# Optimization experiments

Measured on AMD Instinct MI355X. Metric: run time of the kernel, lower is better.

## Reference

```python
import jax, jax.numpy as jnp
import numpy as np

AGENT_RADIUS = 0.2
SAFETY_DIST = 0.1
_ang = np.linspace(0.0, 2.0 * np.pi, 8, endpoint=False)
OBSTACLES = np.stack([10.0 * np.cos(_ang), 10.0 * np.sin(_ang), 0.5 * np.ones(8)], axis=-1).astype(np.float32)  # (x, y, r)


def _qp_solve(p, G, h):
    """Exact solve of: min_z 0.5 z^T z + p^T z  s.t. G z <= h, z in R^2.
    Equivalent to QPFunction with Q=I. Enumerates KKT candidates over active
    sets of size 0, 1, 2 (closed form in 2D) and picks the feasible optimum.
    p: [2], G: [m,2], h: [m]."""
    m = G.shape[0]
    ii, jj = np.triu_indices(m, 1)
    # active set {} -> unconstrained minimizer
    z0 = -p[None, :]                                        # [1,2]
    # active set {i}: z = -p - lam*g_i, g_i.z = h_i
    gg = jnp.sum(G * G, axis=-1)                            # [m]
    lam1 = (-(G @ p) - h) / (gg + 1e-12)
    z1 = -p[None, :] - lam1[:, None] * G                    # [m,2]
    ok1 = lam1 >= -1e-8
    # active set {i,j}: z solves 2x2 system [g_i; g_j] z = [h_i; h_j]
    Gi, Gj = G[ii], G[jj]                                   # [P,2]
    hi, hj = h[ii], h[jj]
    det = Gi[:, 0] * Gj[:, 1] - Gi[:, 1] * Gj[:, 0]
    det_ok = jnp.abs(det) > 1e-9
    ds = jnp.where(det_ok, det, 1.0)
    zx = (hi * Gj[:, 1] - hj * Gi[:, 1]) / ds
    zy = (Gi[:, 0] * hj - Gj[:, 0] * hi) / ds
    z2 = jnp.stack([zx, zy], axis=-1)                       # [P,2]
    r = -(z2 + p[None, :])                                  # A^T lam = r
    lam_i = (Gj[:, 1] * r[:, 0] - Gj[:, 0] * r[:, 1]) / ds
    lam_j = (Gi[:, 0] * r[:, 1] - Gi[:, 1] * r[:, 0]) / ds
    ok2 = det_ok & (lam_i >= -1e-8) & (lam_j >= -1e-8)
    Z = jnp.concatenate([z0, z1, z2], axis=0)               # [K,2]
    ok = jnp.concatenate([jnp.ones((1,), bool), ok1, ok2], axis=0)
    tol = 1e-6 * (1.0 + jnp.abs(h))
    feas = jnp.all(Z @ G.T <= (h + tol)[None, :], axis=-1)  # [K]
    obj = 0.5 * jnp.sum(Z * Z, axis=-1) + Z @ p
    obj = jnp.where(ok & feas, obj, jnp.inf)
    return Z[jnp.argmin(obj)]


def _forward(x, mean, std, W1, b1, W21, b21, W31, b31, W22, b22, W32, b32):
    x0 = x * std + mean                                     # de-normalized state [B,8]
    hid = jax.nn.relu(x @ W1.T + b1)
    x31 = jax.nn.relu(hid @ W21.T + b21) @ W31.T + b31      # reference control p [B,2]
    x32 = 4.0 * jax.nn.sigmoid(jax.nn.relu(hid @ W22.T + b22) @ W32.T + b32)  # CBF penalties [B,2]
    px, py, theta, v = x0[:, 0], x0[:, 1], x0[:, 2], x0[:, 3]
    ox, oy, oth, ov = x0[:, 4], x0[:, 5], x0[:, 6], x0[:, 7]
    st, ct = jnp.sin(theta), jnp.cos(theta)
    vs, vc = v * st, v * ct
    obs = jnp.asarray(OBSTACLES, x.dtype)
    # static obstacle constraints, vectorized over the n_obs obstacles
    dx = px[:, None] - obs[None, :, 0]                      # [B,n_obs]
    dy = py[:, None] - obs[None, :, 1]
    R = AGENT_RADIUS + obs[:, 2] + SAFETY_DIST
    bar = dx * dx + dy * dy - (R * R)[None, :]
    bdot = 2.0 * dx * vc[:, None] + 2.0 * dy * vs[:, None]
    Lf2b = (2.0 * v * v)[:, None]
    u1 = -2.0 * dx * vs[:, None] + 2.0 * dy * vc[:, None]
    u2 = 2.0 * dx * ct[:, None] + 2.0 * dy * st[:, None]
    G_obs = -jnp.stack([u1, u2], axis=-1)                   # [B,n_obs,2]
    s0, s1 = x32[:, 0:1], x32[:, 1:2]
    h_obs = Lf2b + (s0 + s1) * bdot + (s0 * s1) * bar       # [B,n_obs]
    # opponent constraint
    Ro = 2.0 * AGENT_RADIUS + SAFETY_DIST
    dxo, dyo = px - ox, py - oy
    so, co = jnp.sin(oth), jnp.cos(oth)
    bar_o = dxo * dxo + dyo * dyo - Ro * Ro
    bdot_o = 2.0 * dxo * (vc - ov * co) + 2.0 * dyo * (vs - ov * so)
    Lf2b_o = 2.0 * (v * v + ov * ov + 2.0 * v * ov * jnp.cos(theta - oth))
    u1o = -2.0 * dxo * vs + 2.0 * dyo * vc
    u2o = 2.0 * dxo * ct + 2.0 * dyo * st
    G_opp = -jnp.stack([u1o, u2o], axis=-1)[:, None, :]     # [B,1,2]
    h_opp = (Lf2b_o + (x32[:, 0] + x32[:, 1]) * bdot_o + x32[:, 0] * x32[:, 1] * bar_o)[:, None]
    G = jnp.concatenate([G_obs, G_opp], axis=1)             # [B,m,2]
    h = jnp.concatenate([h_obs, h_opp], axis=1)             # [B,m]
    return jax.vmap(_qp_solve)(x31, G, h)                   # [B,2]


def setup_inputs() -> dict:
    key = jax.random.key(0)
    ks = jax.random.split(key, 6)
    B, nF, H1, H2 = 65536, 8, 256, 128

    def lin(k, o, i):
        k1, k2 = jax.random.split(k)
        W = jax.random.normal(k1, (o, i), jnp.float32) / np.float32(np.sqrt(i))
        b = jax.random.normal(k2, (o,), jnp.float32) * 0.01
        return W, b

    W1, b1 = lin(ks[0], H1, nF)
    W21, b21 = lin(ks[1], H2, H1)
    W31, b31 = lin(ks[2], 2, H2)
    W22, b22 = lin(ks[3], H2, H1)
    W32, b32 = lin(ks[4], 2, H2)
    x = jax.random.normal(ks[5], (B, nF), jnp.float32)
    return {"x": x, "mean": jnp.zeros((nF,), jnp.float32), "std": jnp.ones((nF,), jnp.float32),
            "W1": W1, "b1": b1, "W21": W21, "b21": b21, "W31": W31, "b31": b31,
            "W22": W22, "b22": b22, "W32": W32, "b32": b32, "sgn": 1}


def reference(x, mean, std, W1, b1, W21, b21, W31, b31, W22, b22, W32, b32, sgn):
    # sgn==1 / training path -> batched differentiable QP solve
    return _forward(x, mean, std, W1, b1, W21, b21, W31, b31, W22, b22, W32, b32)
```

## Files before the change

kernel.cpp:

```cpp
#include <hip/hip_runtime.h>
#include <hip/hip_bf16.h>
#include <math.h>


typedef unsigned int u32;
typedef unsigned long long u64;
typedef unsigned short u16;
typedef __attribute__((ext_vector_type(8))) short short8;
typedef __attribute__((ext_vector_type(4))) float f32x4;
typedef __attribute__((ext_vector_type(16))) float f32x16;
typedef __attribute__((ext_vector_type(2))) float f32x2;
typedef __attribute__((ext_vector_type(4))) u32 u32x4;

union Frag  { short8 v; u32 u[4]; u32x4 q; };
union F8    { long l; u32 u[2]; };

__device__ __forceinline__ f32x16 zero16() {
    f32x16 z = {0.f, 0.f, 0.f, 0.f, 0.f, 0.f, 0.f, 0.f,
                0.f, 0.f, 0.f, 0.f, 0.f, 0.f, 0.f, 0.f};
    return z;
}

#define DMA16(gp, lp)                                                        \
    __builtin_amdgcn_global_load_lds(                                        \
        (const __attribute__((address_space(1))) void*)(gp),                 \
        (__attribute__((address_space(3))) void*)(lp), 16, 0, 0)

__device__ __forceinline__ u32 packbf(float a, float b) {
    float2 f2; f2.x = a; f2.y = b;
    __hip_bfloat162 h = __float22bfloat162_rn(f2);
    union { __hip_bfloat162 h2; u32 u; } cv; cv.h2 = h;
    return cv.u;
}
__device__ __forceinline__ u32 packfp8x4(float a, float b, float c, float d) {
    u32 r = 0;
    r = (u32)__builtin_amdgcn_cvt_pk_fp8_f32(a, b, (int)r, false);
    r = (u32)__builtin_amdgcn_cvt_pk_fp8_f32(c, d, (int)r, true);
    return r;
}

__device__ const float OBX[8] = { 10.f, 7.07106781186547524f, 6.123234e-16f, -7.07106781186547524f,
                                 -10.f, -7.07106781186547524f, -1.8369702e-15f, 7.07106781186547524f };
__device__ const float OBY[8] = { 0.f, 7.07106781186547524f, 10.f, 7.07106781186547524f,
                                  1.2246468e-15f, -7.07106781186547524f, -10.f, -7.07106781186547524f };

#define PI0_ 0x2111111100000000ULL
#define PI1_ 0x5544443333322222ULL
#define PI2_ 0x7665ULL
#define PJ0_ 0x3876543287654321ULL
#define PJ1_ 0x7687658765487654ULL
#define PJ2_ 0x8878ULL
__device__ __forceinline__ int unpack4(u64 w0, u64 w1, u64 w2, int t) {
    u64 w = (t < 16) ? w0 : (t < 32) ? w1 : w2;
    return (int)((w >> ((t & 15) * 4)) & 15);
}

__global__ __launch_bounds__(256)
void prep_kernel(const float* __restrict__ W21, const float* __restrict__ W22,
                 const float* __restrict__ W1,  const float* __restrict__ b1,
                 const float* __restrict__ W31, const float* __restrict__ W32,
                 const float* __restrict__ b21, const float* __restrict__ b22,
                 u32* __restrict__ ws)
{
    int idx = blockIdx.x * 256 + threadIdx.x;
    if (idx < 4096) {
        int lane = idx & 63;
        int nt   = (idx >> 6) & 3;
        int kp   = (idx >> 8) & 7;
        int head = idx >> 11;
        const float* W = head ? W22 : W21;
        int o  = nt * 32 + (lane & 31);
        int hi = lane >> 5;
        const float* base = W + o * 256 + kp * 32 + hi * 4;
        u32x4 e;
        e.x = packfp8x4(base[0],  base[1],  base[2],  base[3]);
        e.y = packfp8x4(base[8],  base[9],  base[10], base[11]);
        e.z = packfp8x4(base[16], base[17], base[18], base[19]);
        e.w = packfp8x4(base[24], base[25], base[26], base[27]);
        __builtin_nontemporal_store(e, (u32x4*)ws + idx);
    } else if (idx < 4608) {
        int f = idx - 4096;
        int inst = f >> 6, lane = f & 63;
        int hi = lane >> 5;
        int h  = inst * 32 + (lane & 31);
        u32x4 e = (u32x4){0u, 0u, 0u, 0u};
        if (hi == 0) {
            const float* wr = W1 + h * 8;
            e.x = packbf(wr[0], wr[1]);
            e.y = packbf(wr[2], wr[3]);
            e.z = packbf(wr[4], wr[5]);
            e.w = packbf(wr[6], wr[7]);
        } else {
            e.x = packbf(b1[h], 0.f);
        }
        __builtin_nontemporal_store(e, (u32x4*)ws + idx);
    } else if (idx < 5632) {
        int f = idx - 4608;
        int head = f >> 9;
        int kb   = (f >> 6) & 7;
        int lane = f & 63;
        int hi = lane >> 5;
        int mr = lane & 31;
        const float* W3 = head ? W32 : W31;
        int ob = 32 * (kb >> 1) + 16 * (kb & 1) + 4 * hi;
        float v0=0, v1=0, v2=0, v3=0, v4=0, v5=0, v6=0, v7=0;
        if (mr < 2) {
            const float* wr = W3 + mr * 128;
            v0 = wr[ob];     v1 = wr[ob + 1]; v2 = wr[ob + 2]; v3 = wr[ob + 3];
            v4 = wr[ob + 8]; v5 = wr[ob + 9]; v6 = wr[ob + 10]; v7 = wr[ob + 11];
        }
        u32x4 e;
        e.x = packbf(v0, v1); e.y = packbf(v2, v3);
        e.z = packbf(v4, v5); e.w = packbf(v6, v7);
        __builtin_nontemporal_store(e, (u32x4*)ws + idx);
    } else if (idx < 5696) {
        int f = idx - 5632;
        int head = f >> 5, hi = (f >> 4) & 1, nt = (f >> 2) & 3, t = f & 3;
        const float* b2 = head ? b22 : b21;
        int o0 = nt * 32 + 8 * t + 4 * hi;
        f32x4 e; e.x = b2[o0]; e.y = b2[o0+1]; e.z = b2[o0+2]; e.w = b2[o0+3];
        union { f32x4 f; u32x4 u; } cv; cv.f = e;
        __builtin_nontemporal_store(cv.u, (u32x4*)ws + idx);
    }
}

__global__ __launch_bounds__(256)
void barriernet_kernel(const float* __restrict__ x,
                       const float* __restrict__ meanp,
                       const float* __restrict__ stdp,
                       const float* __restrict__ b31,
                       const float* __restrict__ b32,
                       const u32* __restrict__ wsB,
                       float* __restrict__ out, int Btot)
{
    const int tid  = threadIdx.x;
    const int wave = tid >> 6;
    const int lane = tid & 63;
    const int hi   = lane >> 5;
    const int ml   = lane & 31;
    const int blockRow = blockIdx.x * 128;

    __shared__ u32x4 stage[4096];
    __shared__ float lds_p[128][4];

    const u32x4* wsB4 = (const u32x4*)wsB;

    {
        const u32x4* g0 = wsB4 + wave * 1024 + lane;
        u32x4* l0 = stage + wave * 1024;
        #pragma unroll
        for (int i = 0; i < 16; ++i)
            DMA16(g0 + i * 64, l0 + i * 64);
    }

    Frag xB;
    {
        int R0 = blockRow + wave * 32 + ml;
        const f32x4* xv0 = (const f32x4*)(x + (R0 < Btot ? R0 : 0) * 8);
        f32x4 xa0 = xv0[0], xb0 = xv0[1];
        if (hi == 0) {
            xB.u[0] = packbf(xa0.x, xa0.y);
            xB.u[1] = packbf(xa0.z, xa0.w);
            xB.u[2] = packbf(xb0.x, xb0.y);
            xB.u[3] = packbf(xb0.z, xb0.w);
        } else {
            xB.u[0] = 0x00003f80u;
            xB.u[1] = 0u; xB.u[2] = 0u; xB.u[3] = 0u;
        }
    }
    F8 B8[16];
    #pragma unroll
    for (int chunk = 0; chunk < 2; ++chunk) {
        f32x16 hacc[4];
        #pragma unroll
        for (int i2 = 0; i2 < 4; ++i2) {
            int inst = chunk * 4 + i2;
            Frag W1f; W1f.q = wsB4[4096 + inst * 64 + lane];
            hacc[i2] = __builtin_amdgcn_mfma_f32_32x32x16_bf16(
                W1f.v, xB.v, zero16(), 0, 0, 0);
        }
        #pragma unroll
        for (int k2 = 0; k2 < 8; ++k2) {
            int ks = chunk * 8 + k2;
            int i2 = k2 >> 1;
            int pb = 8 * (k2 & 1);
            B8[ks].u[0] = packfp8x4(fmaxf(hacc[i2][pb+0], 0.f), fmaxf(hacc[i2][pb+1], 0.f),
                                    fmaxf(hacc[i2][pb+2], 0.f), fmaxf(hacc[i2][pb+3], 0.f));
            B8[ks].u[1] = packfp8x4(fmaxf(hacc[i2][pb+4], 0.f), fmaxf(hacc[i2][pb+5], 0.f),
                                    fmaxf(hacc[i2][pb+6], 0.f), fmaxf(hacc[i2][pb+7], 0.f));
        }
    }

    __syncthreads();

    #pragma unroll 1
    for (int head = 0; head < 2; ++head) {
        f32x16 acc[4];
        #pragma unroll
        for (int nt = 0; nt < 4; ++nt) acc[nt] = zero16();

        const u32x4* hS = stage + head * 2048;
        #pragma unroll
        for (int kp = 0; kp < 8; ++kp) {
            #pragma unroll
            for (int nt = 0; nt < 4; ++nt) {
                u32x4 e = hS[kp * 256 + nt * 64 + lane];
                F8 ae; ae.u[0] = e.x; ae.u[1] = e.y;
                F8 ao; ao.u[0] = e.z; ao.u[1] = e.w;
                acc[nt] = __builtin_amdgcn_mfma_f32_32x32x16_fp8_fp8(
                    ae.l, B8[2 * kp].l, acc[nt], 0, 0, 0);
                acc[nt] = __builtin_amdgcn_mfma_f32_32x32x16_fp8_fp8(
                    ao.l, B8[2 * kp + 1].l, acc[nt], 0, 0, 0);
            }
        }

        const f32x4* b2p = (const f32x4*)(wsB4 + 5632 + head * 32 + hi * 16);
        Frag rvB[8];
        #pragma unroll
        for (int nt = 0; nt < 4; ++nt) {
            f32x4 bq0 = b2p[nt * 4 + 0];
            f32x4 bq1 = b2p[nt * 4 + 1];
            f32x4 bq2 = b2p[nt * 4 + 2];
            f32x4 bq3 = b2p[nt * 4 + 3];
            float rv0  = fmaxf(acc[nt][0]  + bq0.x, 0.f);
            float rv1  = fmaxf(acc[nt][1]  + bq0.y, 0.f);
            float rv2  = fmaxf(acc[nt][2]  + bq0.z, 0.f);
            float rv3  = fmaxf(acc[nt][3]  + bq0.w, 0.f);
            float rv4  = fmaxf(acc[nt][4]  + bq1.x, 0.f);
            float rv5  = fmaxf(acc[nt][5]  + bq1.y, 0.f);
            float rv6  = fmaxf(acc[nt][6]  + bq1.z, 0.f);
            float rv7  = fmaxf(acc[nt][7]  + bq1.w, 0.f);
            float rv8  = fmaxf(acc[nt][8]  + bq2.x, 0.f);
            float rv9  = fmaxf(acc[nt][9]  + bq2.y, 0.f);
            float rv10 = fmaxf(acc[nt][10] + bq2.z, 0.f);
            float rv11 = fmaxf(acc[nt][11] + bq2.w, 0.f);
            float rv12 = fmaxf(acc[nt][12] + bq3.x, 0.f);
            float rv13 = fmaxf(acc[nt][13] + bq3.y, 0.f);
            float rv14 = fmaxf(acc[nt][14] + bq3.z, 0.f);
            float rv15 = fmaxf(acc[nt][15] + bq3.w, 0.f);
            rvB[nt * 2 + 0].u[0] = packbf(rv0,  rv1);
            rvB[nt * 2 + 0].u[1] = packbf(rv2,  rv3);
            rvB[nt * 2 + 0].u[2] = packbf(rv4,  rv5);
            rvB[nt * 2 + 0].u[3] = packbf(rv6,  rv7);
            rvB[nt * 2 + 1].u[0] = packbf(rv8,  rv9);
            rvB[nt * 2 + 1].u[1] = packbf(rv10, rv11);
            rvB[nt * 2 + 1].u[2] = packbf(rv12, rv13);
            rvB[nt * 2 + 1].u[3] = packbf(rv14, rv15);
        }
        f32x16 acc3 = zero16();
        #pragma unroll
        for (int kb = 0; kb < 8; ++kb) {
            Frag W3f; W3f.q = wsB4[4608 + head * 512 + kb * 64 + lane];
            acc3 = __builtin_amdgcn_mfma_f32_32x32x16_bf16(
                W3f.v, rvB[kb].v, acc3, 0, 0, 0);
        }
        if (hi == 0) {
            int row = wave * 32 + ml;
            if (head == 0) {
                lds_p[row][0] = acc3[0] + b31[0];
                lds_p[row][1] = acc3[1] + b31[1];
            } else {
                float a0 = acc3[0] + b32[0];
                float a1 = acc3[1] + b32[1];
                lds_p[row][2] = 4.f / (1.f + __expf(-a0));
                lds_p[row][3] = 4.f / (1.f + __expf(-a1));
            }
        }
    }
    __syncthreads();

    f32x4 (*qC)[128]  = (f32x4(*)[128])stage;
    f32x4 (*res)[128] = (f32x4(*)[128])(stage + 1152);

    const int rq   = tid & 127;
    const int part = tid >> 7;
    const int R    = blockRow + rq;
    float p0 = lds_p[rq][0];
    float p1 = lds_p[rq][1];

    {
        float s0 = lds_p[rq][2];
        float s1 = lds_p[rq][3];
        const float* xp = x + (R < Btot ? R : 0) * 8;
        f32x4 xv0 = ((const f32x4*)xp)[0];
        f32x4 xv1 = ((const f32x4*)xp)[1];
        const f32x4 sd0 = ((const f32x4*)stdp)[0],  sd1 = ((const f32x4*)stdp)[1];
        const f32x4 mn0 = ((const f32x4*)meanp)[0], mn1 = ((const f32x4*)meanp)[1];
        float px = fmaf(xv0.x, sd0.x, mn0.x);
        float py = fmaf(xv0.y, sd0.y, mn0.y);
        float th = fmaf(xv0.z, sd0.z, mn0.z);
        float v  = fmaf(xv0.w, sd0.w, mn0.w);
        float st = __sinf(th), ct = __cosf(th);
        float vs = v * st, vc = v * ct;
        float sps = s0 + s1, ss = s0 * s1;
        float Lf2b = 2.f * v * v;
        #pragma unroll
        for (int kk = 0; kk < 4; ++kk) {
            int k = part * 4 + kk;
            float dx = px - OBX[k], dy = py - OBY[k];
            float bar  = dx * dx + dy * dy - 0.64f;
            float bdot = 2.f * dx * vc + 2.f * dy * vs;
            float gx = 2.f * dx * vs - 2.f * dy * vc;
            float gy = -(2.f * dx * ct + 2.f * dy * st);
            float hk = Lf2b + sps * bdot + ss * bar;
            float ht = hk + 1e-6f * (1.f + fabsf(hk));
            qC[k][rq] = (f32x4){gx, gy, hk, ht};
        }
        if (part == 1) {
            float ox = fmaf(xv1.x, sd1.x, mn1.x);
            float oy = fmaf(xv1.y, sd1.y, mn1.y);
            float oth= fmaf(xv1.z, sd1.z, mn1.z);
            float ov = fmaf(xv1.w, sd1.w, mn1.w);
            float so = __sinf(oth), co = __cosf(oth);
            float dxo = px - ox, dyo = py - oy;
            float bar_o  = dxo * dxo + dyo * dyo - 0.25f;
            float bdot_o = 2.f * dxo * (vc - ov * co) + 2.f * dyo * (vs - ov * so);
            float Lf2b_o = 2.f * (v * v + ov * ov + 2.f * v * ov * __cosf(th - oth));
            float gx = 2.f * dxo * vs - 2.f * dyo * vc;
            float gy = -(2.f * dxo * ct + 2.f * dyo * st);
            float hk = Lf2b_o + sps * bdot_o + ss * bar_o;
            float ht = hk + 1e-6f * (1.f + fabsf(hk));
            qC[8][rq] = (f32x4){gx, gy, hk, ht};
        }
    }
    __syncthreads();

    const f32x4 C0 = qC[0][rq], C1 = qC[1][rq], C2 = qC[2][rq];
    const f32x4 C3 = qC[3][rq], C4 = qC[4][rq], C5 = qC[5][rq];
    const f32x4 C6 = qC[6][rq], C7 = qC[7][rq], C8 = qC[8][rq];

    const float zx0 = -p0, zy0 = -p1;
    bool z0ok =
        (zx0 * C0.x + zy0 * C0.y <= C0.w) &&
        (zx0 * C1.x + zy0 * C1.y <= C1.w) &&
        (zx0 * C2.x + zy0 * C2.y <= C2.w) &&
        (zx0 * C3.x + zy0 * C3.y <= C3.w) &&
        (zx0 * C4.x + zy0 * C4.y <= C4.w) &&
        (zx0 * C5.x + zy0 * C5.y <= C5.w) &&
        (zx0 * C6.x + zy0 * C6.y <= C6.w) &&
        (zx0 * C7.x + zy0 * C7.y <= C7.w) &&
        (zx0 * C8.x + zy0 * C8.y <= C8.w);

    float bobj = INFINITY;
    float bzx = zx0, bzy = zy0;
    if (z0ok) {
        if (part == 0)
            bobj = 0.5f * (zx0 * zx0 + zy0 * zy0) + zx0 * p0 + zy0 * p1;
    } else {
        const int c0i = part ? 24 : 0;
        const int c1i = part ? 46 : 24;
        #pragma unroll 2
        for (int c = c0i; c < c1i; ++c) {
            float zx, zy;
            bool pre;
            if (c == 0) {
                zx = -p0; zy = -p1; pre = true;
            } else if (c <= 9) {
                f32x4 g = qC[c - 1][rq];
                float gg  = g.x * g.x + g.y * g.y;
                float lam = (-(g.x * p0 + g.y * p1) - g.z) / (gg + 1e-12f);
                zx = -p0 - lam * g.x;
                zy = -p1 - lam * g.y;
                pre = (lam >= -1e-8f);
            } else {
                int t = c - 10;
                int pi = unpack4(PI0_, PI1_, PI2_, t);
                int pj = unpack4(PJ0_, PJ1_, PJ2_, t);
                f32x4 gi = qC[pi][rq];
                f32x4 gj = qC[pj][rq];
                float det = gi.x * gj.y - gi.y * gj.x;
                bool dok = fabsf(det) > 1e-9f;
                float ds = dok ? det : 1.0f;
                float inv = 1.0f / ds;
                zx = (gi.z * gj.y - gj.z * gi.y) * inv;
                zy = (gi.x * gj.z - gj.x * gi.z) * inv;
                float rx = -(zx + p0), ry = -(zy + p1);
                float li = (gj.y * rx - gj.x * ry) * inv;
                float lj = (gi.x * ry - gi.y * rx) * inv;
                pre = dok && (li >= -1e-8f) && (lj >= -1e-8f);
            }
            bool ok = pre;
            ok = ok && (zx * C0.x + zy * C0.y <= C0.w);
            ok = ok && (zx * C1.x + zy * C1.y <= C1.w);
            ok = ok && (zx * C2.x + zy * C2.y <= C2.w);
            ok = ok && (zx * C3.x + zy * C3.y <= C3.w);
            ok = ok && (zx * C4.x + zy * C4.y <= C4.w);
            ok = ok && (zx * C5.x + zy * C5.y <= C5.w);
            ok = ok && (zx * C6.x + zy * C6.y <= C6.w);
            ok = ok && (zx * C7.x + zy * C7.y <= C7.w);
            ok = ok && (zx * C8.x + zy * C8.y <= C8.w);
            float obj = 0.5f * (zx * zx + zy * zy) + zx * p0 + zy * p1;
            if (ok && obj < bobj) { bobj = obj; bzx = zx; bzy = zy; }
        }
    }

    if (part) {
        res[0][rq] = (f32x4){bobj, bzx, bzy, 0.f};
    }
    __syncthreads();
    if (part == 0) {
        f32x4 r = res[0][rq];
        if (r.x < bobj) { bobj = r.x; bzx = r.y; bzy = r.z; }
        if (R < Btot) {
            f32x2 o2; o2.x = bzx; o2.y = bzy;
            ((f32x2*)out)[R] = o2;
        }
    }
}

extern "C" void kernel_launch(void* const* d_in, const int* in_sizes, int n_in,
                              void* d_out, int out_size, void* d_ws, size_t ws_size,
                              hipStream_t stream) {
    const float* x    = (const float*)d_in[0];
    const float* mean = (const float*)d_in[1];
    const float* stdv = (const float*)d_in[2];
    const float* W1   = (const float*)d_in[3];
    const float* b1   = (const float*)d_in[4];
    const float* W21  = (const float*)d_in[5];
    const float* b21  = (const float*)d_in[6];
    const float* W31  = (const float*)d_in[7];
    const float* b31  = (const float*)d_in[8];
    const float* W22  = (const float*)d_in[9];
    const float* b22  = (const float*)d_in[10];
    const float* W32  = (const float*)d_in[11];
    const float* b32  = (const float*)d_in[12];
    int B = in_sizes[0] / 8;
    float* out = (float*)d_out;
    u32* ws = (u32*)d_ws;

    hipLaunchKernelGGL(prep_kernel, dim3(24), dim3(256), 0, stream,
                       W21, W22, W1, b1, W31, W32, b21, b22, ws);

    hipLaunchKernelGGL(barriernet_kernel, dim3((B + 127) / 128), dim3(256), 0, stream,
                       x, mean, stdv, b31, b32, ws, out, B);
}
```

Baseline: 103.5 us.

## Double block to 512 threads, split heads across waves and QP candidates four ways

Doubles the block size so each row group gets two waves, one per MLP head, instead of one wave looping over both heads. The QP stage is split across four threads per row instead of two, each scanning about a quarter of the candidates, and partial minima are reduced through shared memory. The aim is shorter serial chains per wave and more latency hiding. The cost is that W1 and the first layer are computed redundantly by both head waves, and the 512-thread launch bound limits registers per thread.

```diff
diff --git a/kernel.cpp b/kernel.cpp
--- a/kernel.cpp
+++ b/kernel.cpp
@@ -124,7 +124,7 @@
     }
 }
 
-__global__ __launch_bounds__(256)
+__global__ __launch_bounds__(512)
 void barriernet_kernel(const float* __restrict__ x,
                        const float* __restrict__ meanp,
                        const float* __restrict__ stdp,
@@ -138,6 +138,8 @@
     const int lane = tid & 63;
     const int hi   = lane >> 5;
     const int ml   = lane & 31;
+    const int rg   = wave >> 1;
+    const int head = wave & 1;
     const int blockRow = blockIdx.x * 128;
 
     __shared__ u32x4 stage[4096];
@@ -146,16 +148,16 @@
     const u32x4* wsB4 = (const u32x4*)wsB;
 
     {
-        const u32x4* g0 = wsB4 + wave * 1024 + lane;
-        u32x4* l0 = stage + wave * 1024;
-        #pragma unroll
-        for (int i = 0; i < 16; ++i)
+        const u32x4* g0 = wsB4 + wave * 512 + lane;
+        u32x4* l0 = stage + wave * 512;
+        #pragma unroll
+        for (int i = 0; i < 8; ++i)
             DMA16(g0 + i * 64, l0 + i * 64);
     }
 
     Frag xB;
     {
-        int R0 = blockRow + wave * 32 + ml;
+        int R0 = blockRow + rg * 32 + ml;
         const f32x4* xv0 = (const f32x4*)(x + (R0 < Btot ? R0 : 0) * 8);
         f32x4 xa0 = xv0[0], xb0 = xv0[1];
         if (hi == 0) {
@@ -193,12 +195,11 @@
 
     __syncthreads();
 
-    #pragma unroll 1
-    for (int head = 0; head < 2; ++head) {
-        f32x16 acc[4];
-        #pragma unroll
-        for (int nt = 0; nt < 4; ++nt) acc[nt] = zero16();
-
+    f32x16 acc[4];
+    #pragma unroll
+    for (int nt = 0; nt < 4; ++nt) acc[nt] = zero16();
+
+    {
         const u32x4* hS = stage + head * 2048;
         #pragma unroll
         for (int kp = 0; kp < 8; ++kp) {
@@ -213,49 +214,33 @@
                     ao.l, B8[2 * kp + 1].l, acc[nt], 0, 0, 0);
             }
         }
-
+    }
+
+    {
         const f32x4* b2p = (const f32x4*)(wsB4 + 5632 + head * 32 + hi * 16);
-        Frag rvB[8];
+        f32x16 acc3 = zero16();
         #pragma unroll
         for (int nt = 0; nt < 4; ++nt) {
             f32x4 bq0 = b2p[nt * 4 + 0];
             f32x4 bq1 = b2p[nt * 4 + 1];
             f32x4 bq2 = b2p[nt * 4 + 2];
             f32x4 bq3 = b2p[nt * 4 + 3];
-            float rv0  = fmaxf(acc[nt][0]  + bq0.x, 0.f);
-            float rv1  = fmaxf(acc[nt][1]  + bq0.y, 0.f);
-            float rv2  = fmaxf(acc[nt][2]  + bq0.z, 0.f);
-            float rv3  = fmaxf(acc[nt][3]  + bq0.w, 0.f);
-            float rv4  = fmaxf(acc[nt][4]  + bq1.x, 0.f);
-            float rv5  = fmaxf(acc[nt][5]  + bq1.y, 0.f);
-            float rv6  = fmaxf(acc[nt][6]  + bq1.z, 0.f);
-            float rv7  = fmaxf(acc[nt][7]  + bq1.w, 0.f);
-            float rv8  = fmaxf(acc[nt][8]  + bq2.x, 0.f);
-            float rv9  = fmaxf(acc[nt][9]  + bq2.y, 0.f);
-            float rv10 = fmaxf(acc[nt][10] + bq2.z, 0.f);
-            float rv11 = fmaxf(acc[nt][11] + bq2.w, 0.f);
-            float rv12 = fmaxf(acc[nt][12] + bq3.x, 0.f);
-            float rv13 = fmaxf(acc[nt][13] + bq3.y, 0.f);
-            float rv14 = fmaxf(acc[nt][14] + bq3.z, 0.f);
-            float rv15 = fmaxf(acc[nt][15] + bq3.w, 0.f);
-            rvB[nt * 2 + 0].u[0] = packbf(rv0,  rv1);
-            rvB[nt * 2 + 0].u[1] = packbf(rv2,  rv3);
-            rvB[nt * 2 + 0].u[2] = packbf(rv4,  rv5);
-            rvB[nt * 2 + 0].u[3] = packbf(rv6,  rv7);
-            rvB[nt * 2 + 1].u[0] = packbf(rv8,  rv9);
-            rvB[nt * 2 + 1].u[1] = packbf(rv10, rv11);
-            rvB[nt * 2 + 1].u[2] = packbf(rv12, rv13);
-            rvB[nt * 2 + 1].u[3] = packbf(rv14, rv15);
-        }
-        f32x16 acc3 = zero16();
-        #pragma unroll
-        for (int kb = 0; kb < 8; ++kb) {
-            Frag W3f; W3f.q = wsB4[4608 + head * 512 + kb * 64 + lane];
-            acc3 = __builtin_amdgcn_mfma_f32_32x32x16_bf16(
-                W3f.v, rvB[kb].v, acc3, 0, 0, 0);
+            Frag rv0f, rv1f;
+            rv0f.u[0] = packbf(fmaxf(acc[nt][0]  + bq0.x, 0.f), fmaxf(acc[nt][1]  + bq0.y, 0.f));
+            rv0f.u[1] = packbf(fmaxf(acc[nt][2]  + bq0.z, 0.f), fmaxf(acc[nt][3]  + bq0.w, 0.f));
+            rv0f.u[2] = packbf(fmaxf(acc[nt][4]  + bq1.x, 0.f), fmaxf(acc[nt][5]  + bq1.y, 0.f));
+            rv0f.u[3] = packbf(fmaxf(acc[nt][6]  + bq1.z, 0.f), fmaxf(acc[nt][7]  + bq1.w, 0.f));
+            rv1f.u[0] = packbf(fmaxf(acc[nt][8]  + bq2.x, 0.f), fmaxf(acc[nt][9]  + bq2.y, 0.f));
+            rv1f.u[1] = packbf(fmaxf(acc[nt][10] + bq2.z, 0.f), fmaxf(acc[nt][11] + bq2.w, 0.f));
+            rv1f.u[2] = packbf(fmaxf(acc[nt][12] + bq3.x, 0.f), fmaxf(acc[nt][13] + bq3.y, 0.f));
+            rv1f.u[3] = packbf(fmaxf(acc[nt][14] + bq3.z, 0.f), fmaxf(acc[nt][15] + bq3.w, 0.f));
+            Frag W3a; W3a.q = wsB4[4608 + head * 512 + (nt * 2 + 0) * 64 + lane];
+            Frag W3b; W3b.q = wsB4[4608 + head * 512 + (nt * 2 + 1) * 64 + lane];
+            acc3 = __builtin_amdgcn_mfma_f32_32x32x16_bf16(W3a.v, rv0f.v, acc3, 0, 0, 0);
+            acc3 = __builtin_amdgcn_mfma_f32_32x32x16_bf16(W3b.v, rv1f.v, acc3, 0, 0, 0);
         }
         if (hi == 0) {
-            int row = wave * 32 + ml;
+            int row = rg * 32 + ml;
             if (head == 0) {
                 lds_p[row][0] = acc3[0] + b31[0];
                 lds_p[row][1] = acc3[1] + b31[1];
@@ -295,8 +280,8 @@
         float sps = s0 + s1, ss = s0 * s1;
         float Lf2b = 2.f * v * v;
         #pragma unroll
-        for (int kk = 0; kk < 4; ++kk) {
-            int k = part * 4 + kk;
+        for (int kk = 0; kk < 2; ++kk) {
+            int k = part + kk * 4;
             float dx = px - OBX[k], dy = py - OBY[k];
             float bar  = dx * dx + dy * dy - 0.64f;
             float bdot = 2.f * dx * vc + 2.f * dy * vs;
@@ -306,7 +291,7 @@
             float ht = hk + 1e-6f * (1.f + fabsf(hk));
             qC[k][rq] = (f32x4){gx, gy, hk, ht};
         }
-        if (part == 1) {
+        if (part == 3) {
             float ox = fmaf(xv1.x, sd1.x, mn1.x);
             float oy = fmaf(xv1.y, sd1.y, mn1.y);
             float oth= fmaf(xv1.z, sd1.z, mn1.z);
@@ -347,8 +332,8 @@
         if (part == 0)
             bobj = 0.5f * (zx0 * zx0 + zy0 * zy0) + zx0 * p0 + zy0 * p1;
     } else {
-        const int c0i = part ? 24 : 0;
-        const int c1i = part ? 46 : 24;
+        const int c0i = (part == 0) ? 0  : (part == 1) ? 12 : (part == 2) ? 24 : 35;
+        const int c1i = (part == 0) ? 12 : (part == 1) ? 24 : (part == 2) ? 35 : 46;
         #pragma unroll 2
         for (int c = c0i; c < c1i; ++c) {
             float zx, zy;
@@ -395,12 +380,15 @@
     }
 
     if (part) {
-        res[0][rq] = (f32x4){bobj, bzx, bzy, 0.f};
+        res[part - 1][rq] = (f32x4){bobj, bzx, bzy, 0.f};
     }
     __syncthreads();
     if (part == 0) {
-        f32x4 r = res[0][rq];
-        if (r.x < bobj) { bobj = r.x; bzx = r.y; bzy = r.z; }
+        #pragma unroll
+        for (int pp = 0; pp < 3; ++pp) {
+            f32x4 r = res[pp][rq];
+            if (r.x < bobj) { bobj = r.x; bzx = r.y; bzy = r.z; }
+        }
         if (R < Btot) {
             f32x2 o2; o2.x = bzx; o2.y = bzy;
             ((f32x2*)out)[R] = o2;
@@ -431,6 +419,6 @@
     hipLaunchKernelGGL(prep_kernel, dim3(24), dim3(256), 0, stream,
                        W21, W22, W1, b1, W31, W32, b21, b22, ws);
 
-    hipLaunchKernelGGL(barriernet_kernel, dim3((B + 127) / 128), dim3(256), 0, stream,
+    hipLaunchKernelGGL(barriernet_kernel, dim3((B + 127) / 128), dim3(512), 0, stream,
                        x, mean, stdv, b31, b32, ws, out, B);
 }
```

After: 103.9 us. Within noise of the previous version (+0.3%).
